# Kernel tuning notes

Measured on AMD Instinct MI355X. Metric: run time of the kernel, lower is better.

Reference implementation:

```python
import jax, jax.numpy as jnp
import numpy as np

BLOCK = 128  # block_size=(128,128) from MoeFP8Matmul
E, H, I = 8, 2048, 2816  # experts, hidden, intermediate
T, K = 512, 2  # tokens, top-k

_FP8 = getattr(jnp, "float8_e4m3fn", jnp.float32)

def _dequant(w, s):
    # w: [N, Kd] fp8 values (stored fp32), s: [N//128, Kd//128] inverse scales
    s_full = jnp.repeat(jnp.repeat(s, BLOCK, axis=-2), BLOCK, axis=-1)
    return w * s_full

def setup_inputs() -> dict:
    key = jax.random.key(0)
    ks = jax.random.split(key, 7)
    x = jax.random.normal(ks[0], (T, H), dtype=jnp.float32)
    topk_ids = jax.random.randint(ks[1], (T, K), 0, E, dtype=jnp.int64)
    topk_weights = jax.random.uniform(ks[2], (T, K), dtype=jnp.float32)
    # fp8-representable weight values (round-trip through e4m3)
    w13 = (jax.random.normal(ks[3], (E, 2 * I, H), dtype=jnp.float32) * 0.5)
    w13_fp8 = w13.astype(_FP8).astype(jnp.float32)
    w2 = (jax.random.normal(ks[4], (E, H, I), dtype=jnp.float32) * 0.5)
    w2_fp8 = w2.astype(_FP8).astype(jnp.float32)
    w13_scale = jax.random.uniform(ks[5], (E, (2 * I) // BLOCK, H // BLOCK),
                                   dtype=jnp.float32, minval=0.5, maxval=1.5)
    w2_scale = jax.random.uniform(ks[6], (E, H // BLOCK, I // BLOCK),
                                  dtype=jnp.float32, minval=0.5, maxval=1.5)
    return {"x": x, "topk_ids": topk_ids, "topk_weights": topk_weights,
            "w13_fp8": w13_fp8, "w13_scale": w13_scale,
            "w2_fp8": w2_fp8, "w2_scale": w2_scale}

def reference(x, topk_ids, topk_weights, w13_fp8, w13_scale, w2_fp8, w2_scale):
    # Per-expert block-FP8 dequant then grouped SwiGLU MoE GEMM, weighted-summed by router.
    out = jnp.zeros_like(x)
    for e in range(E):  # small fixed expert count
        W13 = _dequant(w13_fp8[e], w13_scale[e])   # [2I, H]
        W2 = _dequant(w2_fp8[e], w2_scale[e])      # [H, I]
        h = x @ W13.T                              # [T, 2I]
        gate, up = jnp.split(h, 2, axis=-1)
        act = jax.nn.silu(gate) * up               # [T, I]
        oe = act @ W2.T                            # [T, H]
        coef = jnp.sum(jnp.where(topk_ids == e, topk_weights, 0.0), axis=-1)  # [T]
        out = out + coef[:, None] * oe
    return out
```

## Files before the change

### kernel.cpp

```cpp
#include <hip/hip_runtime.h>
#include <hip/hip_bf16.h>
#include <cstdint>
#include <cstddef>

#define E_   8
#define H_   2048
#define I_   2816
#define T_   512
#define KK_  2
#define NPAIR (T_*KK_)

#define TM   192
#define TN   64
#define BK   64
#define LDSA 72
#define MT_  3

typedef __attribute__((ext_vector_type(8))) short          bf16x8;
typedef __attribute__((ext_vector_type(4))) float          f32x4;
typedef __attribute__((ext_vector_type(4))) unsigned short u16x4;

__device__ __forceinline__ unsigned short f2bf(float f){
  union { float f; unsigned u; } a; a.f = f;
  unsigned u = a.u;
  unsigned r = u + 0x7fffu + ((u >> 16) & 1u);
  return (unsigned short)(r >> 16);
}

__global__ void route_kernel(const int* __restrict__ ids, const float* __restrict__ w,
                             int* __restrict__ offs, int* __restrict__ ptok,
                             float* __restrict__ pw){
  __shared__ int scnt[E_];
  __shared__ int scur[E_];
  const int tid = threadIdx.x;
  if (tid < E_) scnt[tid] = 0;
  __syncthreads();
  const int e = ids[tid];
  atomicAdd(&scnt[e], 1);
  __syncthreads();
  if (tid == 0){
    int s = 0;
    for (int i = 0; i < E_; i++){ offs[i] = s; scur[i] = s; s += scnt[i]; }
    offs[E_] = s;
  }
  __syncthreads();
  const int pos = atomicAdd(&scur[e], 1);
  ptok[pos] = tid >> 1;
  pw[pos]   = w[tid];
}

__global__ __launch_bounds__(256, 2)
void gemm1_kernel(const float* __restrict__ x, const float* __restrict__ w13,
                  const float* __restrict__ s13, const int* __restrict__ offs,
                  const int* __restrict__ ptok, unsigned short* __restrict__ act)
{
  const int e   = blockIdx.z;
  const int off = offs[e];
  const int cnt = offs[e+1] - off;
  const int m0  = blockIdx.y * TM;
  if (m0 >= cnt) return;
  const int rows = min(TM, cnt - m0);
  const int nb   = blockIdx.x * TN;

  __shared__ __align__(16) unsigned short As[TM][LDSA];
  __shared__ __align__(16) unsigned short Bs[2*TN][LDSA];

  const int tid  = threadIdx.x;
  const int wave = tid >> 6;
  const int lane = tid & 63;
  const int quad = lane >> 4;
  const int l16  = lane & 15;

  const float* w13e = w13 + (size_t)e * (2*I_) * H_;
  const float* s13e = s13 + (size_t)e * (2*I_/128) * (H_/128);

  const int f4   = tid & 15;
  const int rbase = tid >> 4;

  const float* aptr[12];
  #pragma unroll
  for (int t = 0; t < 12; t++){
    const int row = rbase + t*16;
    aptr[t] = (row < rows) ? (x + (size_t)ptok[off + m0 + row] * H_) : nullptr;
  }
  const float* bptr[8];
  int bsrow[8];
  #pragma unroll
  for (int t = 0; t < 8; t++){
    const int r  = rbase + t*16;
    const int gr = (r >> 6)*I_ + nb + (r & 63);
    bptr[t]  = w13e + (size_t)gr * H_;
    bsrow[t] = (gr >> 7)*(H_/128);
  }

  f32x4 acc[2][MT_][4];
  #pragma unroll
  for (int h = 0; h < 2; h++)
    #pragma unroll
    for (int mt = 0; mt < MT_; mt++)
      #pragma unroll
      for (int nt = 0; nt < 4; nt++)
        acc[h][mt][nt] = (f32x4){0.f, 0.f, 0.f, 0.f};

  for (int kb = 0; kb < H_; kb += BK){
    #pragma unroll
    for (int t = 0; t < 12; t++){
      const int row = rbase + t*16;
      u16x4 v4 = (u16x4){0,0,0,0};
      if (aptr[t]){
        float4 v = *(const float4*)(aptr[t] + kb + f4*4);
        v4.x = f2bf(v.x); v4.y = f2bf(v.y); v4.z = f2bf(v.z); v4.w = f2bf(v.w);
      }
      *(u16x4*)&As[row][f4*4] = v4;
    }
    #pragma unroll
    for (int t = 0; t < 8; t++){
      const int r = rbase + t*16;
      const float s = s13e[bsrow[t] + (kb >> 7)];
      float4 v = *(const float4*)(bptr[t] + kb + f4*4);
      u16x4 v4;
      v4.x = f2bf(v.x*s); v4.y = f2bf(v.y*s); v4.z = f2bf(v.z*s); v4.w = f2bf(v.w*s);
      *(u16x4*)&Bs[r][f4*4] = v4;
    }
    __syncthreads();

    #pragma unroll
    for (int kk = 0; kk < BK; kk += 32){
      bf16x8 af[MT_];
      #pragma unroll
      for (int mt = 0; mt < MT_; mt++)
        af[mt] = *(const bf16x8*)&As[wave*48 + mt*16 + l16][kk + quad*8];
      #pragma unroll
      for (int hh = 0; hh < 2; hh++){
        #pragma unroll
        for (int nt = 0; nt < 4; nt++){
          bf16x8 bfv = *(const bf16x8*)&Bs[hh*64 + nt*16 + l16][kk + quad*8];
          #pragma unroll
          for (int mt = 0; mt < MT_; mt++)
            acc[hh][mt][nt] = __builtin_amdgcn_mfma_f32_16x16x32_bf16(af[mt], bfv, acc[hh][mt][nt], 0, 0, 0);
        }
      }
    }
    __syncthreads();
  }

  #pragma unroll
  for (int mt = 0; mt < MT_; mt++){
    #pragma unroll
    for (int nt = 0; nt < 4; nt++){
      #pragma unroll
      for (int r = 0; r < 4; r++){
        const int m = wave*48 + mt*16 + quad*4 + r;
        if (m < rows){
          const float g = acc[0][mt][nt][r];
          const float u = acc[1][mt][nt][r];
          const float sg = g / (1.f + __expf(-g));
          act[(size_t)(off + m0 + m)*I_ + (nb + nt*16 + l16)] = f2bf(sg * u);
        }
      }
    }
  }
}

__global__ __launch_bounds__(256, 2)
void gemm2_kernel(const unsigned short* __restrict__ act, const float* __restrict__ w2,
                  const float* __restrict__ s2, const int* __restrict__ offs,
                  const int* __restrict__ ptok, const float* __restrict__ pw,
                  float* __restrict__ out)
{
  const int e   = blockIdx.z;
  const int off = offs[e];
  const int cnt = offs[e+1] - off;
  const int m0  = blockIdx.y * TM;
  if (m0 >= cnt) return;
  const int rows = min(TM, cnt - m0);
  const int nb   = blockIdx.x * TN;

  __shared__ __align__(16) unsigned short As[TM][LDSA];
  __shared__ __align__(16) unsigned short Bs[TN][LDSA];

  const int tid  = threadIdx.x;
  const int wave = tid >> 6;
  const int lane = tid & 63;
  const int quad = lane >> 4;
  const int l16  = lane & 15;

  const float* w2e = w2 + (size_t)e * H_ * I_;
  const float* s2e = s2 + (size_t)e * (H_/128) * (I_/128);

  const int ch  = tid & 7;
  const int ar8 = tid >> 3;
  const unsigned short* aptr[6];
  #pragma unroll
  for (int t = 0; t < 6; t++){
    const int row = ar8 + t*32;
    aptr[t] = (row < rows) ? (act + (size_t)(off + m0 + row) * I_) : nullptr;
  }
  const int f4    = tid & 15;
  const int rbase = tid >> 4;
  const float* bptr[4];
  int bsrow[4];
  #pragma unroll
  for (int t = 0; t < 4; t++){
    const int gr = nb + rbase + t*16;
    bptr[t]  = w2e + (size_t)gr * I_;
    bsrow[t] = (gr >> 7)*(I_/128);
  }

  f32x4 acc[MT_][4];
  #pragma unroll
  for (int mt = 0; mt < MT_; mt++)
    #pragma unroll
    for (int nt = 0; nt < 4; nt++)
      acc[mt][nt] = (f32x4){0.f, 0.f, 0.f, 0.f};

  for (int kb = 0; kb < I_; kb += BK){
    #pragma unroll
    for (int t = 0; t < 6; t++){
      const int row = ar8 + t*32;
      bf16x8 v = (bf16x8){0,0,0,0,0,0,0,0};
      if (aptr[t]) v = *(const bf16x8*)(aptr[t] + kb + ch*8);
      *(bf16x8*)&As[row][ch*8] = v;
    }
    #pragma unroll
    for (int t = 0; t < 4; t++){
      const int r = rbase + t*16;
      const float s = s2e[bsrow[t] + (kb >> 7)];
      float4 v = *(const float4*)(bptr[t] + kb + f4*4);
      u16x4 v4;
      v4.x = f2bf(v.x*s); v4.y = f2bf(v.y*s); v4.z = f2bf(v.z*s); v4.w = f2bf(v.w*s);
      *(u16x4*)&Bs[r][f4*4] = v4;
    }
    __syncthreads();

    #pragma unroll
    for (int kk = 0; kk < BK; kk += 32){
      bf16x8 af[MT_];
      #pragma unroll
      for (int mt = 0; mt < MT_; mt++)
        af[mt] = *(const bf16x8*)&As[wave*48 + mt*16 + l16][kk + quad*8];
      #pragma unroll
      for (int nt = 0; nt < 4; nt++){
        bf16x8 bfv = *(const bf16x8*)&Bs[nt*16 + l16][kk + quad*8];
        #pragma unroll
        for (int mt = 0; mt < MT_; mt++)
          acc[mt][nt] = __builtin_amdgcn_mfma_f32_16x16x32_bf16(af[mt], bfv, acc[mt][nt], 0, 0, 0);
      }
    }
    __syncthreads();
  }

  #pragma unroll
  for (int mt = 0; mt < MT_; mt++){
    #pragma unroll
    for (int nt = 0; nt < 4; nt++){
      #pragma unroll
      for (int r = 0; r < 4; r++){
        const int m = wave*48 + mt*16 + quad*4 + r;
        if (m < rows){
          const int p = off + m0 + m;
          const float coef = pw[p];
          const int t = ptok[p];
          atomicAdd(&out[(size_t)t*H_ + nb + nt*16 + l16], coef * acc[mt][nt][r]);
        }
      }
    }
  }
}

extern "C" void kernel_launch(void* const* d_in, const int* in_sizes, int n_in,
                              void* d_out, int out_size, void* d_ws, size_t ws_size,
                              hipStream_t stream){
  const float* x   = (const float*)d_in[0];
  const int*   ids = (const int*)  d_in[1];
  const float* tw  = (const float*)d_in[2];
  const float* w13 = (const float*)d_in[3];
  const float* s13 = (const float*)d_in[4];
  const float* w2  = (const float*)d_in[5];
  const float* s2  = (const float*)d_in[6];
  float* out = (float*)d_out;

  char* ws = (char*)d_ws;
  int*   offs = (int*)ws;
  int*   ptok = (int*)(ws + 64);
  float* pw   = (float*)(ws + 64 + NPAIR*4);
  unsigned short* act = (unsigned short*)(ws + 16384);

  hipMemsetAsync(d_out, 0, (size_t)T_*H_*sizeof(float), stream);
  route_kernel<<<1, NPAIR, 0, stream>>>(ids, tw, offs, ptok, pw);
  gemm1_kernel<<<dim3(I_/TN, (NPAIR + TM - 1)/TM, E_), 256, 0, stream>>>(x, w13, s13, offs, ptok, act);
  gemm2_kernel<<<dim3(H_/TN, (NPAIR + TM - 1)/TM, E_), 256, 0, stream>>>(act, w2, s2, offs, ptok, pw, out);
}
```

Baseline: 814.8 us.

## Pre-gather bf16 activations, double-buffer weight tiles, replace atomics with combine pass

```diff
diff --git a/kernel.cpp b/kernel.cpp
--- a/kernel.cpp
+++ b/kernel.cpp
@@ -7,18 +7,17 @@
 #define H_   2048
 #define I_   2816
 #define T_   512
-#define KK_  2
-#define NPAIR (T_*KK_)
+#define NPAIR 1024
 
 #define TM   192
-#define TN   64
+#define TN   32
 #define BK   64
-#define LDSA 72
+#define LDSB 72
 #define MT_  3
 
 typedef __attribute__((ext_vector_type(8))) short          bf16x8;
 typedef __attribute__((ext_vector_type(4))) float          f32x4;
-typedef __attribute__((ext_vector_type(4))) unsigned short u16x4;
+typedef __attribute__((ext_vector_type(8))) unsigned short u16x8;
 
 __device__ __forceinline__ unsigned short f2bf(float f){
   union { float f; unsigned u; } a; a.f = f;
@@ -27,9 +26,9 @@
   return (unsigned short)(r >> 16);
 }
 
-__global__ void route_kernel(const int* __restrict__ ids, const float* __restrict__ w,
+__global__ void route_kernel(const int* __restrict__ ids,
                              int* __restrict__ offs, int* __restrict__ ptok,
-                             float* __restrict__ pw){
+                             int* __restrict__ sop){
   __shared__ int scnt[E_];
   __shared__ int scur[E_];
   const int tid = threadIdx.x;
@@ -46,13 +45,26 @@
   __syncthreads();
   const int pos = atomicAdd(&scur[e], 1);
   ptok[pos] = tid >> 1;
-  pw[pos]   = w[tid];
-}
-
-__global__ __launch_bounds__(256, 2)
-void gemm1_kernel(const float* __restrict__ x, const float* __restrict__ w13,
+  sop[tid]  = pos;
+}
+
+__global__ void prep_kernel(const float* __restrict__ x, const int* __restrict__ ptok,
+                            unsigned short* __restrict__ xg){
+  const int slot = blockIdx.x;
+  const int tok  = ptok[slot];
+  const int k0   = threadIdx.x * 8;
+  const float4 v0 = *(const float4*)(x + (size_t)tok*H_ + k0);
+  const float4 v1 = *(const float4*)(x + (size_t)tok*H_ + k0 + 4);
+  u16x8 o;
+  o[0]=f2bf(v0.x); o[1]=f2bf(v0.y); o[2]=f2bf(v0.z); o[3]=f2bf(v0.w);
+  o[4]=f2bf(v1.x); o[5]=f2bf(v1.y); o[6]=f2bf(v1.z); o[7]=f2bf(v1.w);
+  *(u16x8*)(xg + (size_t)slot*H_ + k0) = o;
+}
+
+__global__ __launch_bounds__(256, 3)
+void gemm1_kernel(const unsigned short* __restrict__ xg, const float* __restrict__ w13,
                   const float* __restrict__ s13, const int* __restrict__ offs,
-                  const int* __restrict__ ptok, unsigned short* __restrict__ act)
+                  unsigned short* __restrict__ act)
 {
   const int e   = blockIdx.z;
   const int off = offs[e];
@@ -62,8 +74,7 @@
   const int rows = min(TM, cnt - m0);
   const int nb   = blockIdx.x * TN;
 
-  __shared__ __align__(16) unsigned short As[TM][LDSA];
-  __shared__ __align__(16) unsigned short Bs[2*TN][LDSA];
+  __shared__ __align__(16) unsigned short Bs[2][2*TN][LDSB];
 
   const int tid  = threadIdx.x;
   const int wave = tid >> 6;
@@ -74,83 +85,92 @@
   const float* w13e = w13 + (size_t)e * (2*I_) * H_;
   const float* s13e = s13 + (size_t)e * (2*I_/128) * (H_/128);
 
-  const int f4   = tid & 15;
-  const int rbase = tid >> 4;
-
-  const float* aptr[12];
-  #pragma unroll
-  for (int t = 0; t < 12; t++){
-    const int row = rbase + t*16;
-    aptr[t] = (row < rows) ? (x + (size_t)ptok[off + m0 + row] * H_) : nullptr;
-  }
-  const float* bptr[8];
-  int bsrow[8];
-  #pragma unroll
-  for (int t = 0; t < 8; t++){
-    const int r  = rbase + t*16;
-    const int gr = (r >> 6)*I_ + nb + (r & 63);
-    bptr[t]  = w13e + (size_t)gr * H_;
-    bsrow[t] = (gr >> 7)*(H_/128);
-  }
-
-  f32x4 acc[2][MT_][4];
+  const int br = tid >> 2;
+  const int bc = tid & 3;
+  const int grow = (br < TN) ? (nb + br) : (I_ + nb + (br - TN));
+  const float* bp = w13e + (size_t)grow * H_;
+  const int srow  = ((br < TN) ? 0 : (I_/128)) + (nb >> 7);
+
+  const unsigned short* aP[MT_];
+  #pragma unroll
+  for (int mt = 0; mt < MT_; mt++){
+    int sl = off + m0 + wave*(TM/4) + mt*16 + l16;
+    sl = min(sl, NPAIR - 1);
+    aP[mt] = xg + (size_t)sl * H_;
+  }
+
+  f32x4 acc[2][MT_][2];
   #pragma unroll
   for (int h = 0; h < 2; h++)
     #pragma unroll
     for (int mt = 0; mt < MT_; mt++)
       #pragma unroll
-      for (int nt = 0; nt < 4; nt++)
+      for (int nt = 0; nt < 2; nt++)
         acc[h][mt][nt] = (f32x4){0.f, 0.f, 0.f, 0.f};
 
+  float4 pb[4];
+  #pragma unroll
+  for (int j = 0; j < 4; j++) pb[j] = *(const float4*)(bp + (bc*4 + j)*4);
+  {
+    const float s = s13e[srow*(H_/128)];
+    u16x8 wv0, wv1;
+    wv0[0]=f2bf(pb[0].x*s); wv0[1]=f2bf(pb[0].y*s); wv0[2]=f2bf(pb[0].z*s); wv0[3]=f2bf(pb[0].w*s);
+    wv0[4]=f2bf(pb[1].x*s); wv0[5]=f2bf(pb[1].y*s); wv0[6]=f2bf(pb[1].z*s); wv0[7]=f2bf(pb[1].w*s);
+    wv1[0]=f2bf(pb[2].x*s); wv1[1]=f2bf(pb[2].y*s); wv1[2]=f2bf(pb[2].z*s); wv1[3]=f2bf(pb[2].w*s);
+    wv1[4]=f2bf(pb[3].x*s); wv1[5]=f2bf(pb[3].y*s); wv1[6]=f2bf(pb[3].z*s); wv1[7]=f2bf(pb[3].w*s);
+    *(u16x8*)&Bs[0][br][bc*16]     = wv0;
+    *(u16x8*)&Bs[0][br][bc*16 + 8] = wv1;
+  }
+  __syncthreads();
+
+  int cur = 0;
   for (int kb = 0; kb < H_; kb += BK){
-    #pragma unroll
-    for (int t = 0; t < 12; t++){
-      const int row = rbase + t*16;
-      u16x4 v4 = (u16x4){0,0,0,0};
-      if (aptr[t]){
-        float4 v = *(const float4*)(aptr[t] + kb + f4*4);
-        v4.x = f2bf(v.x); v4.y = f2bf(v.y); v4.z = f2bf(v.z); v4.w = f2bf(v.w);
-      }
-      *(u16x4*)&As[row][f4*4] = v4;
-    }
-    #pragma unroll
-    for (int t = 0; t < 8; t++){
-      const int r = rbase + t*16;
-      const float s = s13e[bsrow[t] + (kb >> 7)];
-      float4 v = *(const float4*)(bptr[t] + kb + f4*4);
-      u16x4 v4;
-      v4.x = f2bf(v.x*s); v4.y = f2bf(v.y*s); v4.z = f2bf(v.z*s); v4.w = f2bf(v.w*s);
-      *(u16x4*)&Bs[r][f4*4] = v4;
-    }
-    __syncthreads();
-
-    #pragma unroll
-    for (int kk = 0; kk < BK; kk += 32){
-      bf16x8 af[MT_];
+    const bool more = (kb + BK) < H_;
+    if (more){
+      #pragma unroll
+      for (int j = 0; j < 4; j++) pb[j] = *(const float4*)(bp + kb + BK + (bc*4 + j)*4);
+    }
+    bf16x8 af[2][MT_];
+    #pragma unroll
+    for (int kk = 0; kk < 2; kk++)
       #pragma unroll
       for (int mt = 0; mt < MT_; mt++)
-        af[mt] = *(const bf16x8*)&As[wave*48 + mt*16 + l16][kk + quad*8];
+        af[kk][mt] = *(const bf16x8*)(aP[mt] + kb + kk*32 + quad*8);
+
+    #pragma unroll
+    for (int kk = 0; kk < 2; kk++){
       #pragma unroll
       for (int hh = 0; hh < 2; hh++){
         #pragma unroll
-        for (int nt = 0; nt < 4; nt++){
-          bf16x8 bfv = *(const bf16x8*)&Bs[hh*64 + nt*16 + l16][kk + quad*8];
+        for (int nt = 0; nt < 2; nt++){
+          bf16x8 bv = *(const bf16x8*)&Bs[cur][hh*TN + nt*16 + l16][kk*32 + quad*8];
           #pragma unroll
           for (int mt = 0; mt < MT_; mt++)
-            acc[hh][mt][nt] = __builtin_amdgcn_mfma_f32_16x16x32_bf16(af[mt], bfv, acc[hh][mt][nt], 0, 0, 0);
+            acc[hh][mt][nt] = __builtin_amdgcn_mfma_f32_16x16x32_bf16(af[kk][mt], bv, acc[hh][mt][nt], 0, 0, 0);
         }
       }
     }
-    __syncthreads();
+    if (more){
+      const float s = s13e[srow*(H_/128) + ((kb + BK) >> 7)];
+      u16x8 wv0, wv1;
+      wv0[0]=f2bf(pb[0].x*s); wv0[1]=f2bf(pb[0].y*s); wv0[2]=f2bf(pb[0].z*s); wv0[3]=f2bf(pb[0].w*s);
+      wv0[4]=f2bf(pb[1].x*s); wv0[5]=f2bf(pb[1].y*s); wv0[6]=f2bf(pb[1].z*s); wv0[7]=f2bf(pb[1].w*s);
+      wv1[0]=f2bf(pb[2].x*s); wv1[1]=f2bf(pb[2].y*s); wv1[2]=f2bf(pb[2].z*s); wv1[3]=f2bf(pb[2].w*s);
+      wv1[4]=f2bf(pb[3].x*s); wv1[5]=f2bf(pb[3].y*s); wv1[6]=f2bf(pb[3].z*s); wv1[7]=f2bf(pb[3].w*s);
+      *(u16x8*)&Bs[cur^1][br][bc*16]     = wv0;
+      *(u16x8*)&Bs[cur^1][br][bc*16 + 8] = wv1;
+      __syncthreads();
+      cur ^= 1;
+    }
   }
 
   #pragma unroll
   for (int mt = 0; mt < MT_; mt++){
     #pragma unroll
-    for (int nt = 0; nt < 4; nt++){
+    for (int nt = 0; nt < 2; nt++){
       #pragma unroll
       for (int r = 0; r < 4; r++){
-        const int m = wave*48 + mt*16 + quad*4 + r;
+        const int m = wave*(TM/4) + mt*16 + quad*4 + r;
         if (m < rows){
           const float g = acc[0][mt][nt][r];
           const float u = acc[1][mt][nt][r];
@@ -162,11 +182,10 @@
   }
 }
 
-__global__ __launch_bounds__(256, 2)
+__global__ __launch_bounds__(256, 4)
 void gemm2_kernel(const unsigned short* __restrict__ act, const float* __restrict__ w2,
                   const float* __restrict__ s2, const int* __restrict__ offs,
-                  const int* __restrict__ ptok, const float* __restrict__ pw,
-                  float* __restrict__ out)
+                  float* __restrict__ buf)
 {
   const int e   = blockIdx.z;
   const int off = offs[e];
@@ -176,8 +195,7 @@
   const int rows = min(TM, cnt - m0);
   const int nb   = blockIdx.x * TN;
 
-  __shared__ __align__(16) unsigned short As[TM][LDSA];
-  __shared__ __align__(16) unsigned short Bs[TN][LDSA];
+  __shared__ __align__(16) unsigned short Bs[2][TN][LDSB];
 
   const int tid  = threadIdx.x;
   const int wave = tid >> 6;
@@ -188,84 +206,102 @@
   const float* w2e = w2 + (size_t)e * H_ * I_;
   const float* s2e = s2 + (size_t)e * (H_/128) * (I_/128);
 
-  const int ch  = tid & 7;
-  const int ar8 = tid >> 3;
-  const unsigned short* aptr[6];
-  #pragma unroll
-  for (int t = 0; t < 6; t++){
-    const int row = ar8 + t*32;
-    aptr[t] = (row < rows) ? (act + (size_t)(off + m0 + row) * I_) : nullptr;
-  }
-  const int f4    = tid & 15;
-  const int rbase = tid >> 4;
-  const float* bptr[4];
-  int bsrow[4];
-  #pragma unroll
-  for (int t = 0; t < 4; t++){
-    const int gr = nb + rbase + t*16;
-    bptr[t]  = w2e + (size_t)gr * I_;
-    bsrow[t] = (gr >> 7)*(I_/128);
-  }
-
-  f32x4 acc[MT_][4];
+  const int br = tid >> 3;
+  const int bc = tid & 7;
+  const float* bp = w2e + (size_t)(nb + br) * I_;
+  const int srow  = nb >> 7;
+
+  const unsigned short* aP[MT_];
+  #pragma unroll
+  for (int mt = 0; mt < MT_; mt++){
+    int sl = off + m0 + wave*(TM/4) + mt*16 + l16;
+    sl = min(sl, NPAIR - 1);
+    aP[mt] = act + (size_t)sl * I_;
+  }
+
+  f32x4 acc[MT_][2];
   #pragma unroll
   for (int mt = 0; mt < MT_; mt++)
     #pragma unroll
-    for (int nt = 0; nt < 4; nt++)
+    for (int nt = 0; nt < 2; nt++)
       acc[mt][nt] = (f32x4){0.f, 0.f, 0.f, 0.f};
 
+  float4 pb[2];
+  #pragma unroll
+  for (int j = 0; j < 2; j++) pb[j] = *(const float4*)(bp + (bc*2 + j)*4);
+  {
+    const float s = s2e[srow*(I_/128)];
+    u16x8 wv;
+    wv[0]=f2bf(pb[0].x*s); wv[1]=f2bf(pb[0].y*s); wv[2]=f2bf(pb[0].z*s); wv[3]=f2bf(pb[0].w*s);
+    wv[4]=f2bf(pb[1].x*s); wv[5]=f2bf(pb[1].y*s); wv[6]=f2bf(pb[1].z*s); wv[7]=f2bf(pb[1].w*s);
+    *(u16x8*)&Bs[0][br][bc*8] = wv;
+  }
+  __syncthreads();
+
+  int cur = 0;
   for (int kb = 0; kb < I_; kb += BK){
-    #pragma unroll
-    for (int t = 0; t < 6; t++){
-      const int row = ar8 + t*32;
-      bf16x8 v = (bf16x8){0,0,0,0,0,0,0,0};
-      if (aptr[t]) v = *(const bf16x8*)(aptr[t] + kb + ch*8);
-      *(bf16x8*)&As[row][ch*8] = v;
-    }
-    #pragma unroll
-    for (int t = 0; t < 4; t++){
-      const int r = rbase + t*16;
-      const float s = s2e[bsrow[t] + (kb >> 7)];
-      float4 v = *(const float4*)(bptr[t] + kb + f4*4);
-      u16x4 v4;
-      v4.x = f2bf(v.x*s); v4.y = f2bf(v.y*s); v4.z = f2bf(v.z*s); v4.w = f2bf(v.w*s);
-      *(u16x4*)&Bs[r][f4*4] = v4;
-    }
-    __syncthreads();
-
-    #pragma unroll
-    for (int kk = 0; kk < BK; kk += 32){
-      bf16x8 af[MT_];
+    const bool more = (kb + BK) < I_;
+    if (more){
+      #pragma unroll
+      for (int j = 0; j < 2; j++) pb[j] = *(const float4*)(bp + kb + BK + (bc*2 + j)*4);
+    }
+    bf16x8 af[2][MT_];
+    #pragma unroll
+    for (int kk = 0; kk < 2; kk++)
       #pragma unroll
       for (int mt = 0; mt < MT_; mt++)
-        af[mt] = *(const bf16x8*)&As[wave*48 + mt*16 + l16][kk + quad*8];
-      #pragma unroll
-      for (int nt = 0; nt < 4; nt++){
-        bf16x8 bfv = *(const bf16x8*)&Bs[nt*16 + l16][kk + quad*8];
+        af[kk][mt] = *(const bf16x8*)(aP[mt] + kb + kk*32 + quad*8);
+
+    #pragma unroll
+    for (int kk = 0; kk < 2; kk++){
+      #pragma unroll
+      for (int nt = 0; nt < 2; nt++){
+        bf16x8 bv = *(const bf16x8*)&Bs[cur][nt*16 + l16][kk*32 + quad*8];
         #pragma unroll
         for (int mt = 0; mt < MT_; mt++)
-          acc[mt][nt] = __builtin_amdgcn_mfma_f32_16x16x32_bf16(af[mt], bfv, acc[mt][nt], 0, 0, 0);
+          acc[mt][nt] = __builtin_amdgcn_mfma_f32_16x16x32_bf16(af[kk][mt], bv, acc[mt][nt], 0, 0, 0);
       }
     }
-    __syncthreads();
+    if (more){
+      const float s = s2e[srow*(I_/128) + ((kb + BK) >> 7)];
+      u16x8 wv;
+      wv[0]=f2bf(pb[0].x*s); wv[1]=f2bf(pb[0].y*s); wv[2]=f2bf(pb[0].z*s); wv[3]=f2bf(pb[0].w*s);
+      wv[4]=f2bf(pb[1].x*s); wv[5]=f2bf(pb[1].y*s); wv[6]=f2bf(pb[1].z*s); wv[7]=f2bf(pb[1].w*s);
+      *(u16x8*)&Bs[cur^1][br][bc*8] = wv;
+      __syncthreads();
+      cur ^= 1;
+    }
   }
 
   #pragma unroll
   for (int mt = 0; mt < MT_; mt++){
     #pragma unroll
-    for (int nt = 0; nt < 4; nt++){
+    for (int nt = 0; nt < 2; nt++){
       #pragma unroll
       for (int r = 0; r < 4; r++){
-        const int m = wave*48 + mt*16 + quad*4 + r;
-        if (m < rows){
-          const int p = off + m0 + m;
-          const float coef = pw[p];
-          const int t = ptok[p];
-          atomicAdd(&out[(size_t)t*H_ + nb + nt*16 + l16], coef * acc[mt][nt][r]);
-        }
+        const int m = wave*(TM/4) + mt*16 + quad*4 + r;
+        if (m < rows)
+          buf[(size_t)(off + m0 + m)*H_ + (nb + nt*16 + l16)] = acc[mt][nt][r];
       }
     }
   }
+}
+
+__global__ void combine_kernel(const float* __restrict__ buf, const int* __restrict__ sop,
+                               const float* __restrict__ tw, float* __restrict__ out){
+  const int gid = blockIdx.x*256 + threadIdx.x;
+  const int t = gid >> 9;
+  const int c = gid & 511;
+  const int s0 = sop[2*t], s1 = sop[2*t+1];
+  const float w0 = tw[2*t], w1 = tw[2*t+1];
+  const float4 v0 = ((const float4*)buf)[(size_t)s0*(H_/4) + c];
+  const float4 v1 = ((const float4*)buf)[(size_t)s1*(H_/4) + c];
+  float4 o;
+  o.x = w0*v0.x + w1*v1.x;
+  o.y = w0*v0.y + w1*v1.y;
+  o.z = w0*v0.z + w1*v1.z;
+  o.w = w0*v0.w + w1*v1.w;
+  ((float4*)out)[gid] = o;
 }
 
 extern "C" void kernel_launch(void* const* d_in, const int* in_sizes, int n_in,
@@ -281,13 +317,16 @@
   float* out = (float*)d_out;
 
   char* ws = (char*)d_ws;
-  int*   offs = (int*)ws;
-  int*   ptok = (int*)(ws + 64);
-  float* pw   = (float*)(ws + 64 + NPAIR*4);
-  unsigned short* act = (unsigned short*)(ws + 16384);
-
-  hipMemsetAsync(d_out, 0, (size_t)T_*H_*sizeof(float), stream);
-  route_kernel<<<1, NPAIR, 0, stream>>>(ids, tw, offs, ptok, pw);
-  gemm1_kernel<<<dim3(I_/TN, (NPAIR + TM - 1)/TM, E_), 256, 0, stream>>>(x, w13, s13, offs, ptok, act);
-  gemm2_kernel<<<dim3(H_/TN, (NPAIR + TM - 1)/TM, E_), 256, 0, stream>>>(act, w2, s2, offs, ptok, pw, out);
-}
+  int* offs = (int*)ws;
+  int* ptok = (int*)(ws + 64);
+  int* sop  = (int*)(ws + 64 + 4096);
+  unsigned short* xg  = (unsigned short*)(ws + 16384);
+  float*          buf = (float*)(ws + 16384);
+  unsigned short* act = (unsigned short*)(ws + 16384 + (size_t)NPAIR*H_*4);
+
+  route_kernel  <<<1, NPAIR, 0, stream>>>(ids, offs, ptok, sop);
+  prep_kernel   <<<NPAIR, 256, 0, stream>>>(x, ptok, xg);
+  gemm1_kernel  <<<dim3(I_/TN, (NPAIR + TM - 1)/TM, E_), 256, 0, stream>>>(xg, w13, s13, offs, act);
+  gemm2_kernel  <<<dim3(H_/TN, (NPAIR + TM - 1)/TM, E_), 256, 0, stream>>>(act, w2, s2, offs, buf);
+  combine_kernel<<<(T_*H_/4)/256, 256, 0, stream>>>(buf, sop, tw, out);
+}
```

Measured after the change: 793.0 us. 2.7% less time.
